# Optimization experiments

Hardware: AMD Instinct MI355X
Metric: run time of the kernel (lower is better)

Reference implementation:

```python
import jax, jax.numpy as jnp
import numpy as np

D_MODEL = 512
N_HEADS = 8
B, S = 4, 1024
REL_HIDDEN = 64


def setup_inputs() -> dict:
    key = jax.random.key(0)
    ks = jax.random.split(key, 16)

    def g(k, shape, scale=0.02):
        return jax.random.normal(k, shape, dtype=jnp.float32) * scale

    x = jax.random.normal(ks[0], (B, S, D_MODEL), dtype=jnp.float32)
    freqs = jax.random.uniform(ks[1], (B, S, 1), dtype=jnp.float32)
    return {
        "x": x,
        "freqs": freqs,
        "Wq": g(ks[2], (D_MODEL, D_MODEL)), "bq": g(ks[3], (D_MODEL,)),
        "Wk": g(ks[4], (D_MODEL, D_MODEL)), "bk": g(ks[5], (D_MODEL,)),
        "Wv": g(ks[6], (D_MODEL, D_MODEL)), "bv": g(ks[7], (D_MODEL,)),
        "Wo": g(ks[8], (D_MODEL, D_MODEL)), "bo": g(ks[9], (D_MODEL,)),
        "W1": g(ks[10], (2, REL_HIDDEN)), "b1": g(ks[11], (REL_HIDDEN,)),
        "W2": g(ks[12], (REL_HIDDEN, N_HEADS)), "b2": g(ks[13], (N_HEADS,)),
    }


def reference(x, freqs, Wq, bq, Wk, bk, Wv, bv, Wo, bo, W1, b1, W2, b2):
    b, s, d = x.shape
    h = N_HEADS
    dh = d // h

    def proj(W, bias):  # (b,s,d) -> (b,h,s,dh)
        return (x @ W + bias).reshape(b, s, h, dh).transpose(0, 2, 1, 3)

    Q = proj(Wq, bq)
    K = proj(Wk, bk)
    V = proj(Wv, bv)

    scores = jnp.einsum('bhid,bhjd->bhij', Q, K) / jnp.sqrt(jnp.float32(dh))

    # per-pair relative-frequency features: (b,s,s,2)
    eps = 1e-6
    fd = freqs[:, :, None, :] - freqs[:, None, :, :]
    fr = jnp.log((freqs[:, :, None, :] + eps) / (freqs[:, None, :, :] + eps))
    rel = jnp.concatenate([fd, fr], axis=-1)

    # MLP bias -> (b,s,s,h) -> (b,h,s,s)
    bias = jax.nn.relu(rel @ W1 + b1) @ W2 + b2
    scores = scores + jnp.transpose(bias, (0, 3, 1, 2))

    attn = jax.nn.softmax(scores, axis=-1)
    ctx = jnp.einsum('bhij,bhjd->bhid', attn, V)
    ctx = ctx.transpose(0, 2, 1, 3).reshape(b, s, d)
    return ctx @ Wo + bo
```

## Files before the change

### kernel.cpp

```cpp
#include <hip/hip_runtime.h>
#include <hip/hip_bf16.h>
#include <cstdint>

#define BATCH   4
#define SEQ     1024
#define DM      512
#define NH      8
#define DH      64
#define RH      64

typedef float f32x4 __attribute__((ext_vector_type(4)));
typedef __bf16 bf16x8 __attribute__((ext_vector_type(8)));

#define QB_OFF    (0)
#define KB_OFF    (4  << 20)
#define VT_OFF    (8  << 20)
#define XB_OFF    (12 << 20)
#define WT_OFF    (16 << 20)
#define WOT_OFF   (18 << 20)
#define W2T_OFF   (19 << 20)
#define AW_OFF    (20 << 20)
#define CW_OFF    (21 << 20)
#define CTXB_OFF  (22 << 20)
#define BIAS_OFF  (32 << 20)

__global__ __launch_bounds__(256) void cast_x(
    const float* __restrict__ x, __bf16* __restrict__ xb)
{
    const size_t i = ((size_t)blockIdx.x * 256 + threadIdx.x) * 8;
    const float4 a = *(const float4*)&x[i];
    const float4 b = *(const float4*)&x[i + 4];
    bf16x8 o;
    o[0] = (__bf16)a.x; o[1] = (__bf16)a.y; o[2] = (__bf16)a.z; o[3] = (__bf16)a.w;
    o[4] = (__bf16)b.x; o[5] = (__bf16)b.y; o[6] = (__bf16)b.z; o[7] = (__bf16)b.w;
    *(bf16x8*)&xb[i] = o;
}

__global__ __launch_bounds__(256) void cast_w(
    const float* __restrict__ Wq, const float* __restrict__ Wk,
    const float* __restrict__ Wv, const float* __restrict__ Wo,
    __bf16* __restrict__ Wt, __bf16* __restrict__ Wot)
{
    const int t = threadIdx.x;
    const int k0 = blockIdx.x * 64;
    const int n0 = blockIdx.y * 64;
    const int z  = blockIdx.z;
    const float* __restrict__ src = (z == 0) ? Wq : (z == 1) ? Wk : (z == 2) ? Wv : Wo;
    __bf16* __restrict__ dst = (z < 3) ? (Wt + (size_t)(z * 512 + n0) * 512)
                                       : (Wot + (size_t)n0 * 512);

    __shared__ __align__(16) float Ts[64][65];
    #pragma unroll
    for (int i = 0; i < 4; ++i) {
        const int id = t + i * 256;
        const int row = id >> 4, c4 = (id & 15) * 4;
        const float4 v = *(const float4*)&src[(size_t)(k0 + row) * DM + n0 + c4];
        Ts[row][c4 + 0] = v.x; Ts[row][c4 + 1] = v.y;
        Ts[row][c4 + 2] = v.z; Ts[row][c4 + 3] = v.w;
    }
    __syncthreads();
    #pragma unroll
    for (int i = 0; i < 2; ++i) {
        const int id = t + i * 256;
        const int rn = id >> 3, ck = (id & 7) * 8;
        bf16x8 o;
        #pragma unroll
        for (int j = 0; j < 8; ++j) o[j] = (__bf16)Ts[ck + j][rn];
        *(bf16x8*)&dst[(size_t)rn * 512 + k0 + ck] = o;
    }
}

__global__ __launch_bounds__(256) void gemm_qkv_mfma(
    const __bf16* __restrict__ xb, const __bf16* __restrict__ Wt,
    const float* __restrict__ bq, const float* __restrict__ bk,
    const float* __restrict__ bv,
    __bf16* __restrict__ Qb, __bf16* __restrict__ Kb, __bf16* __restrict__ Vtb)
{
    const int t = threadIdx.x;
    const int wave = t >> 6, lane = t & 63;
    const int wm = wave >> 1, wn = wave & 1;
    const int r = lane & 15, kc = lane >> 4, q4 = kc * 4;
    const int lin = blockIdx.y * 12 + blockIdx.x;
    const int swz = (lin & 7) * 48 + (lin >> 3);
    const int m0 = (swz / 12) * 128;
    const int n0 = (swz % 12) * 128;
    const int sec = n0 >> 9;
    const int nn = n0 & 511;

    __shared__ __align__(16) char smem[36864];
    __bf16* __restrict__ As = (__bf16*)smem;
    __bf16* __restrict__ Bs = (__bf16*)(smem + 18432);

    f32x4 acc[4][4];
    #pragma unroll
    for (int i = 0; i < 4; ++i)
        #pragma unroll
        for (int j = 0; j < 4; ++j) acc[i][j] = {0.f, 0.f, 0.f, 0.f};

    const int srow = t >> 3, sck = (t & 7) * 8;
    const __bf16* __restrict__ Ag = xb + (size_t)(m0 + srow) * 512 + sck;
    const __bf16* __restrict__ Bg = Wt + (size_t)(n0 + srow) * 512 + sck;

    for (int k0 = 0; k0 < 512; k0 += 64) {
        bf16x8 ra[4], rb[4];
        #pragma unroll
        for (int i = 0; i < 4; ++i) {
            ra[i] = *(const bf16x8*)(Ag + (size_t)i * 32 * 512 + k0);
            rb[i] = *(const bf16x8*)(Bg + (size_t)i * 32 * 512 + k0);
        }
        __syncthreads();
        #pragma unroll
        for (int i = 0; i < 4; ++i) {
            *(bf16x8*)&As[(srow + i * 32) * 72 + sck] = ra[i];
            *(bf16x8*)&Bs[(srow + i * 32) * 72 + sck] = rb[i];
        }
        __syncthreads();
        #pragma unroll
        for (int ks = 0; ks < 2; ++ks) {
            bf16x8 af[4], bf[4];
            #pragma unroll
            for (int mf = 0; mf < 4; ++mf)
                af[mf] = *(const bf16x8*)&As[(wm * 64 + mf * 16 + r) * 72 + ks * 32 + kc * 8];
            #pragma unroll
            for (int nf = 0; nf < 4; ++nf)
                bf[nf] = *(const bf16x8*)&Bs[(wn * 64 + nf * 16 + r) * 72 + ks * 32 + kc * 8];
            #pragma unroll
            for (int mf = 0; mf < 4; ++mf)
                #pragma unroll
                for (int nf = 0; nf < 4; ++nf)
                    acc[mf][nf] = __builtin_amdgcn_mfma_f32_16x16x32_bf16(
                        af[mf], bf[nf], acc[mf][nf], 0, 0, 0);
        }
    }

    const float* __restrict__ bias = (sec == 0) ? bq : (sec == 1) ? bk : bv;
    __syncthreads();
    __bf16* __restrict__ Ls = (__bf16*)smem;
    if (sec < 2) {
        #pragma unroll
        for (int mf = 0; mf < 4; ++mf)
            #pragma unroll
            for (int nf = 0; nf < 4; ++nf) {
                const int n_l = wn * 64 + nf * 16 + r;
                const float bb = bias[nn + n_l];
                #pragma unroll
                for (int rr = 0; rr < 4; ++rr)
                    Ls[(wm * 64 + mf * 16 + q4 + rr) * 136 + n_l] =
                        (__bf16)(acc[mf][nf][rr] + bb);
            }
    } else {
        #pragma unroll
        for (int mf = 0; mf < 4; ++mf)
            #pragma unroll
            for (int nf = 0; nf < 4; ++nf) {
                const int n_l = wn * 64 + nf * 16 + r;
                const float bb = bias[nn + n_l];
                #pragma unroll
                for (int rr = 0; rr < 4; ++rr)
                    Ls[n_l * 136 + (wm * 64 + mf * 16 + q4 + rr)] =
                        (__bf16)(acc[mf][nf][rr] + bb);
            }
    }
    __syncthreads();

    const int b = m0 >> 10, sbase = m0 & 1023;
    if (sec < 2) {
        __bf16* __restrict__ dst = sec ? Kb : Qb;
        #pragma unroll
        for (int i = 0; i < 8; ++i) {
            const int id = t + i * 256;
            const int row = id >> 4, nc = (id & 15) * 8;
            const bf16x8 v = *(const bf16x8*)&Ls[row * 136 + nc];
            const int ng = nn + nc, h = ng >> 6, c = ng & 63;
            *(bf16x8*)&dst[((size_t)(b * NH + h) * SEQ + sbase + row) * DH + c] = v;
        }
    } else {
        #pragma unroll
        for (int i = 0; i < 8; ++i) {
            const int id = t + i * 256;
            const int nrow = id >> 4, mc = (id & 15) * 8;
            const bf16x8 v = *(const bf16x8*)&Ls[nrow * 136 + mc];
            const int ng = nn + nrow, h = ng >> 6, c = ng & 63;
            *(bf16x8*)&Vtb[((size_t)(b * NH + h) * DH + c) * SEQ + sbase + mc] = v;
        }
    }
}

__global__ __launch_bounds__(256) void gemm_out_mfma(
    const __bf16* __restrict__ ctxb, const __bf16* __restrict__ Wot,
    const float* __restrict__ bo, float* __restrict__ out)
{
    const int t = threadIdx.x;
    const int wave = t >> 6, lane = t & 63;
    const int wm = wave >> 1, wn = wave & 1;
    const int r = lane & 15, kc = lane >> 4, q4 = kc * 4;
    const int lin = blockIdx.y * 4 + blockIdx.x;
    const int swz = (lin & 7) * 16 + (lin >> 3);
    const int m0 = (swz / 4) * 128;
    const int n0 = (swz % 4) * 128;

    __shared__ __align__(16) char smem[36864];
    __bf16* __restrict__ As = (__bf16*)smem;
    __bf16* __restrict__ Bs = (__bf16*)(smem + 18432);

    f32x4 acc[4][4];
    #pragma unroll
    for (int i = 0; i < 4; ++i)
        #pragma unroll
        for (int j = 0; j < 4; ++j) acc[i][j] = {0.f, 0.f, 0.f, 0.f};

    const int srow = t >> 3, sck = (t & 7) * 8;
    const __bf16* __restrict__ Ag = ctxb + (size_t)(m0 + srow) * 512 + sck;
    const __bf16* __restrict__ Bg = Wot + (size_t)(n0 + srow) * 512 + sck;

    for (int k0 = 0; k0 < 512; k0 += 64) {
        bf16x8 ra[4], rb[4];
        #pragma unroll
        for (int i = 0; i < 4; ++i) {
            ra[i] = *(const bf16x8*)(Ag + (size_t)i * 32 * 512 + k0);
            rb[i] = *(const bf16x8*)(Bg + (size_t)i * 32 * 512 + k0);
        }
        __syncthreads();
        #pragma unroll
        for (int i = 0; i < 4; ++i) {
            *(bf16x8*)&As[(srow + i * 32) * 72 + sck] = ra[i];
            *(bf16x8*)&Bs[(srow + i * 32) * 72 + sck] = rb[i];
        }
        __syncthreads();
        #pragma unroll
        for (int ks = 0; ks < 2; ++ks) {
            bf16x8 af[4], bf[4];
            #pragma unroll
            for (int mf = 0; mf < 4; ++mf)
                af[mf] = *(const bf16x8*)&As[(wm * 64 + mf * 16 + r) * 72 + ks * 32 + kc * 8];
            #pragma unroll
            for (int nf = 0; nf < 4; ++nf)
                bf[nf] = *(const bf16x8*)&Bs[(wn * 64 + nf * 16 + r) * 72 + ks * 32 + kc * 8];
            #pragma unroll
            for (int mf = 0; mf < 4; ++mf)
                #pragma unroll
                for (int nf = 0; nf < 4; ++nf)
                    acc[mf][nf] = __builtin_amdgcn_mfma_f32_16x16x32_bf16(
                        af[mf], bf[nf], acc[mf][nf], 0, 0, 0);
        }
    }

    #pragma unroll
    for (int mf = 0; mf < 4; ++mf)
        #pragma unroll
        for (int nf = 0; nf < 4; ++nf) {
            const int n_l = wn * 64 + nf * 16 + r;
            const float bb = bo[n0 + n_l];
            #pragma unroll
            for (int rr = 0; rr < 4; ++rr)
                out[(size_t)(m0 + wm * 64 + mf * 16 + q4 + rr) * DM + n0 + n_l] =
                    acc[mf][nf][rr] + bb;
        }
}

__global__ __launch_bounds__(64) void rel_kernel(
    const float* __restrict__ freqs,
    const float* __restrict__ W1,
    const float* __restrict__ b1,
    const float* __restrict__ W2,
    float* __restrict__ Aw,
    float* __restrict__ Cw,
    __bf16* __restrict__ W2t)
{
    const int row = blockIdx.x;
    const int k = threadIdx.x;
    const float f = freqs[row];
    const float L = logf(f + 1e-6f);
    const float base = f * W1[k] + L * W1[RH + k];
    Aw[(size_t)row * RH + k] = base + b1[k];
    Cw[(size_t)row * RH + k] = -base;
    if (row < 16)
        W2t[row * 64 + k] = (row < NH) ? (__bf16)W2[k * NH + row] : (__bf16)0.f;
}

__global__ __launch_bounds__(256) void bias_mfma(
    const float* __restrict__ Aw, const float* __restrict__ Cw,
    const __bf16* __restrict__ W2t, __bf16* __restrict__ biasb)
{
    const int t = threadIdx.x;
    const int wave = t >> 6, lane = t & 63;
    const int jl = lane & 15, kc = lane >> 4;
    const int j0 = blockIdx.x * 128;
    const int i0 = blockIdx.y * 16;
    const int b  = blockIdx.z;

    __shared__ __align__(16) float Cs[128][68];
    __shared__ __align__(16) __bf16 Lh[4][8][136];

    {
        const int jr = t >> 1, half = (t & 1) * 32;
        const float* __restrict__ src = &Cw[((size_t)b * SEQ + j0 + jr) * RH + half];
        #pragma unroll
        for (int q = 0; q < 8; ++q) {
            const float4 v = *(const float4*)(src + q * 4);
            *(float4*)&Cs[jr][half + q * 4] = v;
        }
    }

    const bf16x8 w2f0 = *(const bf16x8*)&W2t[jl * 64 + kc * 8];
    const bf16x8 w2f1 = *(const bf16x8*)&W2t[jl * 64 + 32 + kc * 8];

    __syncthreads();

    const int h2 = lane >> 3, c8 = (lane & 7) * 8;
    const int iw = i0 + wave * 4;
    #pragma unroll
    for (int ii = 0; ii < 4; ++ii) {
        const int i = iw + ii;
        const float* __restrict__ ap = &Aw[((size_t)b * SEQ + i) * RH];
        const float4 a0 = *(const float4*)(ap + kc * 8);
        const float4 a1 = *(const float4*)(ap + kc * 8 + 4);
        const float4 a2 = *(const float4*)(ap + 32 + kc * 8);
        const float4 a3 = *(const float4*)(ap + 32 + kc * 8 + 4);

        #pragma unroll
        for (int jt = 0; jt < 8; ++jt) {
            const float* __restrict__ cp = &Cs[jt * 16 + jl][kc * 8];
            f32x4 acc = {0.f, 0.f, 0.f, 0.f};

            const float4 c0 = *(const float4*)(cp);
            const float4 c1 = *(const float4*)(cp + 4);
            bf16x8 hb0;
            hb0[0] = (__bf16)fmaxf(a0.x + c0.x, 0.f);
            hb0[1] = (__bf16)fmaxf(a0.y + c0.y, 0.f);
            hb0[2] = (__bf16)fmaxf(a0.z + c0.z, 0.f);
            hb0[3] = (__bf16)fmaxf(a0.w + c0.w, 0.f);
            hb0[4] = (__bf16)fmaxf(a1.x + c1.x, 0.f);
            hb0[5] = (__bf16)fmaxf(a1.y + c1.y, 0.f);
            hb0[6] = (__bf16)fmaxf(a1.z + c1.z, 0.f);
            hb0[7] = (__bf16)fmaxf(a1.w + c1.w, 0.f);
            acc = __builtin_amdgcn_mfma_f32_16x16x32_bf16(w2f0, hb0, acc, 0, 0, 0);

            const float4 c2 = *(const float4*)(cp + 32);
            const float4 c3 = *(const float4*)(cp + 36);
            bf16x8 hb1;
            hb1[0] = (__bf16)fmaxf(a2.x + c2.x, 0.f);
            hb1[1] = (__bf16)fmaxf(a2.y + c2.y, 0.f);
            hb1[2] = (__bf16)fmaxf(a2.z + c2.z, 0.f);
            hb1[3] = (__bf16)fmaxf(a2.w + c2.w, 0.f);
            hb1[4] = (__bf16)fmaxf(a3.x + c3.x, 0.f);
            hb1[5] = (__bf16)fmaxf(a3.y + c3.y, 0.f);
            hb1[6] = (__bf16)fmaxf(a3.z + c3.z, 0.f);
            hb1[7] = (__bf16)fmaxf(a3.w + c3.w, 0.f);
            acc = __builtin_amdgcn_mfma_f32_16x16x32_bf16(w2f1, hb1, acc, 0, 0, 0);

            if (kc < 2) {
                #pragma unroll
                for (int rr = 0; rr < 4; ++rr)
                    Lh[wave][kc * 4 + rr][jt * 16 + jl] = (__bf16)acc[rr];
            }
        }
        asm volatile("s_waitcnt lgkmcnt(0)" ::: "memory");
        const bf16x8 v0 = *(const bf16x8*)&Lh[wave][h2][c8];
        const bf16x8 v1 = *(const bf16x8*)&Lh[wave][h2][64 + c8];
        __bf16* __restrict__ dst =
            &biasb[(((size_t)b * NH + h2) * SEQ + i) * SEQ + j0];
        *(bf16x8*)&dst[c8] = v0;
        *(bf16x8*)&dst[64 + c8] = v1;
    }
}

#define PSTR 1032

__global__ __launch_bounds__(512) void attn_mfma(
    const __bf16* __restrict__ Qb, const __bf16* __restrict__ Kb,
    const __bf16* __restrict__ Vtb, const __bf16* __restrict__ biasb,
    __bf16* __restrict__ ctxb)
{
    const int t = threadIdx.x;
    const int wave = t >> 6, lane = t & 63;
    const int r = lane & 15, kc = lane >> 4;
    const int blk = (blockIdx.x & 7) * 256 + (blockIdx.x >> 3);
    const int it = blk & 63;
    const int h  = (blk >> 6) & 7;
    const int b  = blk >> 9;
    const int s0 = it * 16;
    const int bh = b * NH + h;

    __shared__ __align__(16) __bf16 Pb[16 * PSTR];
    __shared__ __align__(16) float part[1088];
    __shared__ float red[8][16];
    __shared__ float invl[16];

    uint32_t brg[4][8];
    {
        const uint16_t* __restrict__ bb = (const uint16_t*)biasb
            + ((size_t)bh * SEQ + s0 + kc * 4) * SEQ + wave * 128 + r;
        #pragma unroll
        for (int rr = 0; rr < 4; ++rr)
            #pragma unroll
            for (int jt = 0; jt < 8; ++jt)
                brg[rr][jt] = bb[(size_t)rr * SEQ + jt * 16];
    }

    f32x4 sc[8];
    {
        const __bf16* __restrict__ Qp = Qb + ((size_t)bh * SEQ + s0) * DH;
        const __bf16* __restrict__ Kp = Kb + ((size_t)bh * SEQ + wave * 128) * DH;
        const bf16x8 qa0 = *(const bf16x8*)(Qp + r * DH + kc * 8);
        const bf16x8 qa1 = *(const bf16x8*)(Qp + r * DH + 32 + kc * 8);
        __builtin_amdgcn_s_setprio(1);
        #pragma unroll
        for (int jt = 0; jt < 8; ++jt) {
            const bf16x8 kb0 = *(const bf16x8*)(Kp + (size_t)(jt * 16 + r) * DH + kc * 8);
            const bf16x8 kb1 = *(const bf16x8*)(Kp + (size_t)(jt * 16 + r) * DH + 32 + kc * 8);
            f32x4 a = {0.f, 0.f, 0.f, 0.f};
            a = __builtin_amdgcn_mfma_f32_16x16x32_bf16(qa0, kb0, a, 0, 0, 0);
            a = __builtin_amdgcn_mfma_f32_16x16x32_bf16(qa1, kb1, a, 0, 0, 0);
            sc[jt] = a;
        }
        __builtin_amdgcn_s_setprio(0);
    }

    float psum[4] = {0.f, 0.f, 0.f, 0.f};
    #pragma unroll
    for (int jt = 0; jt < 8; ++jt) {
        #pragma unroll
        for (int rr = 0; rr < 4; ++rr) {
            const float s = fmaf(sc[jt][rr], 0.125f,
                                 __uint_as_float(brg[rr][jt] << 16));
            const float p = __expf(fminf(s, 30.f));
            sc[jt][rr] = p;
            psum[rr] += p;
        }
    }
    #pragma unroll
    for (int mask = 8; mask >= 1; mask >>= 1)
        #pragma unroll
        for (int rr = 0; rr < 4; ++rr)
            psum[rr] += __shfl_xor(psum[rr], mask);
    if (r == 0) {
        #pragma unroll
        for (int rr = 0; rr < 4; ++rr) red[wave][kc * 4 + rr] = psum[rr];
    }
    #pragma unroll
    for (int jt = 0; jt < 8; ++jt)
        #pragma unroll
        for (int rr = 0; rr < 4; ++rr)
            Pb[(kc * 4 + rr) * PSTR + wave * 128 + jt * 16 + r] = (__bf16)sc[jt][rr];
    __syncthreads();

    if (t < 16) {
        float l = 0.f;
        #pragma unroll
        for (int w = 0; w < 8; ++w) l += red[w][t];
        invl[t] = 1.0f / l;
    }

    {
        const int ct = wave & 3, kh = wave >> 2;
        const __bf16* __restrict__ Vp =
            Vtb + ((size_t)bh * DH + ct * 16 + r) * SEQ + kh * 512;
        f32x4 acc = {0.f, 0.f, 0.f, 0.f};
        __builtin_amdgcn_s_setprio(1);
        #pragma unroll 4
        for (int jt = 0; jt < 16; ++jt) {
            const bf16x8 pa = *(const bf16x8*)&Pb[r * PSTR + kh * 512 + jt * 32 + kc * 8];
            const bf16x8 vb = *(const bf16x8*)(Vp + jt * 32 + kc * 8);
            acc = __builtin_amdgcn_mfma_f32_16x16x32_bf16(pa, vb, acc, 0, 0, 0);
        }
        __builtin_amdgcn_s_setprio(0);
        if (kh == 1) {
            #pragma unroll
            for (int rr = 0; rr < 4; ++rr)
                part[ct * 272 + (kc * 4 + rr) * 17 + r] = acc[rr];
        }
        __syncthreads();
        if (kh == 0) {
            #pragma unroll
            for (int rr = 0; rr < 4; ++rr) {
                const int row = kc * 4 + rr;
                const float v = (acc[rr] + part[ct * 272 + row * 17 + r]) * invl[row];
                ctxb[((size_t)(b * SEQ) + s0 + row) * DM + h * DH + ct * 16 + r] = (__bf16)v;
            }
        }
    }
}

extern "C" void kernel_launch(void* const* d_in, const int* in_sizes, int n_in,
                              void* d_out, int out_size, void* d_ws, size_t ws_size,
                              hipStream_t stream)
{
    const float* x     = (const float*)d_in[0];
    const float* freqs = (const float*)d_in[1];
    const float* Wq    = (const float*)d_in[2];
    const float* bq    = (const float*)d_in[3];
    const float* Wk    = (const float*)d_in[4];
    const float* bk    = (const float*)d_in[5];
    const float* Wv    = (const float*)d_in[6];
    const float* bv    = (const float*)d_in[7];
    const float* Wo    = (const float*)d_in[8];
    const float* bo    = (const float*)d_in[9];
    const float* W1    = (const float*)d_in[10];
    const float* b1    = (const float*)d_in[11];
    const float* W2    = (const float*)d_in[12];

    char* wsb = (char*)d_ws;
    __bf16* Qb    = (__bf16*)(wsb + QB_OFF);
    __bf16* Kb    = (__bf16*)(wsb + KB_OFF);
    __bf16* Vtb   = (__bf16*)(wsb + VT_OFF);
    __bf16* xb    = (__bf16*)(wsb + XB_OFF);
    __bf16* Wt    = (__bf16*)(wsb + WT_OFF);
    __bf16* Wot   = (__bf16*)(wsb + WOT_OFF);
    __bf16* W2t   = (__bf16*)(wsb + W2T_OFF);
    float*  Aw    = (float*)(wsb + AW_OFF);
    float*  Cw    = (float*)(wsb + CW_OFF);
    __bf16* ctxb  = (__bf16*)(wsb + CTXB_OFF);
    __bf16* biasb = (__bf16*)(wsb + BIAS_OFF);
    float* out = (float*)d_out;

    cast_x<<<dim3(1024), 256, 0, stream>>>(x, xb);
    cast_w<<<dim3(8, 8, 4), 256, 0, stream>>>(Wq, Wk, Wv, Wo, Wt, Wot);
    rel_kernel<<<dim3(4096), 64, 0, stream>>>(freqs, W1, b1, W2, Aw, Cw, W2t);
    gemm_qkv_mfma<<<dim3(12, 32), 256, 0, stream>>>(xb, Wt, bq, bk, bv, Qb, Kb, Vtb);
    bias_mfma<<<dim3(8, 64, 4), 256, 0, stream>>>(Aw, Cw, W2t, biasb);
    attn_mfma<<<dim3(2048), 512, 0, stream>>>(Qb, Kb, Vtb, biasb, ctxb);
    gemm_out_mfma<<<dim3(4, 32), 256, 0, stream>>>(ctxb, Wot, bo, out);
}
```

Measured before the change: 219.5 us.

## Restructure bias MLP kernel to write bias directly without LDS staging

```diff
diff --git a/kernel.cpp b/kernel.cpp
--- a/kernel.cpp
+++ b/kernel.cpp
@@ -284,84 +284,80 @@
 {
     const int t = threadIdx.x;
     const int wave = t >> 6, lane = t & 63;
-    const int jl = lane & 15, kc = lane >> 4;
+    const int il = lane & 15, kc = lane >> 4;
     const int j0 = blockIdx.x * 128;
-    const int i0 = blockIdx.y * 16;
+    const int i0 = blockIdx.y * 32;
     const int b  = blockIdx.z;
 
     __shared__ __align__(16) float Cs[128][68];
-    __shared__ __align__(16) __bf16 Lh[4][8][136];
 
     {
         const int jr = t >> 1, half = (t & 1) * 32;
         const float* __restrict__ src = &Cw[((size_t)b * SEQ + j0 + jr) * RH + half];
         #pragma unroll
-        for (int q = 0; q < 8; ++q) {
-            const float4 v = *(const float4*)(src + q * 4);
-            *(float4*)&Cs[jr][half + q * 4] = v;
-        }
-    }
-
-    const bf16x8 w2f0 = *(const bf16x8*)&W2t[jl * 64 + kc * 8];
-    const bf16x8 w2f1 = *(const bf16x8*)&W2t[jl * 64 + 32 + kc * 8];
-
+        for (int q = 0; q < 8; ++q)
+            *(float4*)&Cs[jr][half + q * 4] = *(const float4*)(src + q * 4);
+    }
+
+    const bf16x8 w2f0 = *(const bf16x8*)&W2t[il * 64 + kc * 8];
+    const bf16x8 w2f1 = *(const bf16x8*)&W2t[il * 64 + 32 + kc * 8];
     __syncthreads();
 
-    const int h2 = lane >> 3, c8 = (lane & 7) * 8;
-    const int iw = i0 + wave * 4;
-    #pragma unroll
-    for (int ii = 0; ii < 4; ++ii) {
-        const int i = iw + ii;
-        const float* __restrict__ ap = &Aw[((size_t)b * SEQ + i) * RH];
+    #pragma unroll
+    for (int ih = 0; ih < 2; ++ih) {
+        const float* __restrict__ ap =
+            &Aw[((size_t)b * SEQ + i0 + ih * 16 + il) * RH];
         const float4 a0 = *(const float4*)(ap + kc * 8);
         const float4 a1 = *(const float4*)(ap + kc * 8 + 4);
         const float4 a2 = *(const float4*)(ap + 32 + kc * 8);
         const float4 a3 = *(const float4*)(ap + 32 + kc * 8 + 4);
 
         #pragma unroll
-        for (int jt = 0; jt < 8; ++jt) {
-            const float* __restrict__ cp = &Cs[jt * 16 + jl][kc * 8];
-            f32x4 acc = {0.f, 0.f, 0.f, 0.f};
-
-            const float4 c0 = *(const float4*)(cp);
-            const float4 c1 = *(const float4*)(cp + 4);
-            bf16x8 hb0;
-            hb0[0] = (__bf16)fmaxf(a0.x + c0.x, 0.f);
-            hb0[1] = (__bf16)fmaxf(a0.y + c0.y, 0.f);
-            hb0[2] = (__bf16)fmaxf(a0.z + c0.z, 0.f);
-            hb0[3] = (__bf16)fmaxf(a0.w + c0.w, 0.f);
-            hb0[4] = (__bf16)fmaxf(a1.x + c1.x, 0.f);
-            hb0[5] = (__bf16)fmaxf(a1.y + c1.y, 0.f);
-            hb0[6] = (__bf16)fmaxf(a1.z + c1.z, 0.f);
-            hb0[7] = (__bf16)fmaxf(a1.w + c1.w, 0.f);
-            acc = __builtin_amdgcn_mfma_f32_16x16x32_bf16(w2f0, hb0, acc, 0, 0, 0);
-
-            const float4 c2 = *(const float4*)(cp + 32);
-            const float4 c3 = *(const float4*)(cp + 36);
-            bf16x8 hb1;
-            hb1[0] = (__bf16)fmaxf(a2.x + c2.x, 0.f);
-            hb1[1] = (__bf16)fmaxf(a2.y + c2.y, 0.f);
-            hb1[2] = (__bf16)fmaxf(a2.z + c2.z, 0.f);
-            hb1[3] = (__bf16)fmaxf(a2.w + c2.w, 0.f);
-            hb1[4] = (__bf16)fmaxf(a3.x + c3.x, 0.f);
-            hb1[5] = (__bf16)fmaxf(a3.y + c3.y, 0.f);
-            hb1[6] = (__bf16)fmaxf(a3.z + c3.z, 0.f);
-            hb1[7] = (__bf16)fmaxf(a3.w + c3.w, 0.f);
-            acc = __builtin_amdgcn_mfma_f32_16x16x32_bf16(w2f1, hb1, acc, 0, 0, 0);
-
-            if (kc < 2) {
+        for (int jb = 0; jb < 4; ++jb) {
+            f32x4 accJ[8];
+            #pragma unroll
+            for (int jj = 0; jj < 8; ++jj) {
+                const float* __restrict__ cp =
+                    &Cs[wave * 32 + jb * 8 + jj][kc * 8];
+                const float4 c0 = *(const float4*)(cp);
+                const float4 c1 = *(const float4*)(cp + 4);
+                const float4 c2 = *(const float4*)(cp + 32);
+                const float4 c3 = *(const float4*)(cp + 36);
+                bf16x8 hb0, hb1;
+                hb0[0] = (__bf16)fmaxf(a0.x + c0.x, 0.f);
+                hb0[1] = (__bf16)fmaxf(a0.y + c0.y, 0.f);
+                hb0[2] = (__bf16)fmaxf(a0.z + c0.z, 0.f);
+                hb0[3] = (__bf16)fmaxf(a0.w + c0.w, 0.f);
+                hb0[4] = (__bf16)fmaxf(a1.x + c1.x, 0.f);
+                hb0[5] = (__bf16)fmaxf(a1.y + c1.y, 0.f);
+                hb0[6] = (__bf16)fmaxf(a1.z + c1.z, 0.f);
+                hb0[7] = (__bf16)fmaxf(a1.w + c1.w, 0.f);
+                hb1[0] = (__bf16)fmaxf(a2.x + c2.x, 0.f);
+                hb1[1] = (__bf16)fmaxf(a2.y + c2.y, 0.f);
+                hb1[2] = (__bf16)fmaxf(a2.z + c2.z, 0.f);
+                hb1[3] = (__bf16)fmaxf(a2.w + c2.w, 0.f);
+                hb1[4] = (__bf16)fmaxf(a3.x + c3.x, 0.f);
+                hb1[5] = (__bf16)fmaxf(a3.y + c3.y, 0.f);
+                hb1[6] = (__bf16)fmaxf(a3.z + c3.z, 0.f);
+                hb1[7] = (__bf16)fmaxf(a3.w + c3.w, 0.f);
+                f32x4 acc = {0.f, 0.f, 0.f, 0.f};
+                acc = __builtin_amdgcn_mfma_f32_16x16x32_bf16(hb0, w2f0, acc, 0, 0, 0);
+                acc = __builtin_amdgcn_mfma_f32_16x16x32_bf16(hb1, w2f1, acc, 0, 0, 0);
+                accJ[jj] = acc;
+            }
+            if (il < 8) {
                 #pragma unroll
-                for (int rr = 0; rr < 4; ++rr)
-                    Lh[wave][kc * 4 + rr][jt * 16 + jl] = (__bf16)acc[rr];
+                for (int rr = 0; rr < 4; ++rr) {
+                    bf16x8 pv;
+                    #pragma unroll
+                    for (int jj = 0; jj < 8; ++jj)
+                        pv[jj] = (__bf16)accJ[jj][rr];
+                    *(bf16x8*)&biasb[(((size_t)b * NH + il) * SEQ
+                                      + i0 + ih * 16 + kc * 4 + rr) * SEQ
+                                     + j0 + wave * 32 + jb * 8] = pv;
+                }
             }
         }
-        asm volatile("s_waitcnt lgkmcnt(0)" ::: "memory");
-        const bf16x8 v0 = *(const bf16x8*)&Lh[wave][h2][c8];
-        const bf16x8 v1 = *(const bf16x8*)&Lh[wave][h2][64 + c8];
-        __bf16* __restrict__ dst =
-            &biasb[(((size_t)b * NH + h2) * SEQ + i) * SEQ + j0];
-        *(bf16x8*)&dst[c8] = v0;
-        *(bf16x8*)&dst[64 + c8] = v1;
     }
 }
 
@@ -518,7 +514,7 @@
     cast_w<<<dim3(8, 8, 4), 256, 0, stream>>>(Wq, Wk, Wv, Wo, Wt, Wot);
     rel_kernel<<<dim3(4096), 64, 0, stream>>>(freqs, W1, b1, W2, Aw, Cw, W2t);
     gemm_qkv_mfma<<<dim3(12, 32), 256, 0, stream>>>(xb, Wt, bq, bk, bv, Qb, Kb, Vtb);
-    bias_mfma<<<dim3(8, 64, 4), 256, 0, stream>>>(Aw, Cw, W2t, biasb);
+    bias_mfma<<<dim3(8, 32, 4), 256, 0, stream>>>(Aw, Cw, W2t, biasb);
     attn_mfma<<<dim3(2048), 512, 0, stream>>>(Qb, Kb, Vtb, biasb, ctxb);
     gemm_out_mfma<<<dim3(4, 32), 256, 0, stream>>>(ctxb, Wot, bo, out);
 }
```

Measured after the change: 223.3 us. No clear change (+1.7%).
